# Kernel tuning notes

Hardware: AMD Instinct MI355X
Metric: run time of the kernel (lower is better)

## Reference

```python
import jax, jax.numpy as jnp
import numpy as np

B, C, H, W = 8, 16, 256, 256
HID = 32

def setup_inputs() -> dict:
    key = jax.random.key(0)
    ks = jax.random.split(key, 6)
    swin_logits = jax.random.normal(ks[0], (B, C, H, W), dtype=jnp.float32)
    gru_logits = jax.random.normal(ks[1], (B, C, H, W), dtype=jnp.float32)
    # per-class gate params (stacked across classes); torch Linear default-ish scale
    W1 = jax.random.normal(ks[2], (C, HID, 2), dtype=jnp.float32) * (1.0 / np.sqrt(2.0))
    b1 = jax.random.normal(ks[3], (C, HID), dtype=jnp.float32) * 0.1
    W2 = jax.random.normal(ks[4], (C, 2, HID), dtype=jnp.float32) * (1.0 / np.sqrt(HID))
    b2 = jax.random.normal(ks[5], (C, 2), dtype=jnp.float32) * 0.1
    # expert_preferences initialized exactly as in the torch module
    pref = np.zeros((C, 2), dtype=np.float32)
    for i in range(C):
        w_hls = 0.3 + 0.4 * (i / max(1, C - 1))
        pref[i] = [w_hls, 1.0 - w_hls]
    expert_preferences = jnp.asarray(pref)
    return {"swin_logits": swin_logits, "gru_logits": gru_logits,
            "W1": W1, "b1": b1, "W2": W2, "b2": b2,
            "expert_preferences": expert_preferences}

def reference(swin_logits, gru_logits, W1, b1, W2, b2, expert_preferences):
    b, c, h, w = swin_logits.shape
    # class-dim softmax over logits
    swin_probs = jax.nn.softmax(swin_logits, axis=1)
    gru_probs = jax.nn.softmax(gru_logits, axis=1)
    # (B,C,H,W) -> (N,C), N = B*H*W
    sp = swin_probs.transpose(0, 2, 3, 1).reshape(-1, c)
    gp = gru_probs.transpose(0, 2, 3, 1).reshape(-1, c)
    gate_in = jnp.stack([sp, gp], axis=-1)  # (N, C, 2)
    # batched per-class gate MLP (Dropout is identity in eval mode)
    hid = jax.nn.relu(jnp.einsum('nci,chi->nch', gate_in, W1) + b1)  # (N,C,HID)
    dynamic_weights = jax.nn.softmax(jnp.einsum('nch,coh->nco', hid, W2) + b2, axis=-1)  # (N,C,2)
    # weighted fusion of expert logits
    sl = swin_logits.transpose(0, 2, 3, 1).reshape(-1, c)
    gl = gru_logits.transpose(0, 2, 3, 1).reshape(-1, c)
    expert_logits = jnp.stack([sl, gl], axis=-1)  # (N,C,2)
    fused_flat = jnp.sum(dynamic_weights * expert_logits, axis=-1)  # (N,C)
    fused_logits = fused_flat.reshape(b, h, w, c).transpose(0, 3, 1, 2)
    return fused_logits, expert_preferences, dynamic_weights
```

## Files before the change

kernel.cpp:

```cpp
#include <hip/hip_runtime.h>

typedef float v2f __attribute__((ext_vector_type(2)));

#define Bc   8
#define Cc   16
#define HWc  65536
#define HIDc 32
#define Npix (Bc * HWc)
#define FUSED_ELEMS (Bc * Cc * HWc)
#define PREF_ELEMS  (Cc * 2)
#define TPB  256
#define WSTRIDE 81
#define PACKED_BYTES (Cc * WSTRIDE * 8)

__global__ void gate_prep(const float* __restrict__ W1, const float* __restrict__ b1,
                          const float* __restrict__ W2, const float* __restrict__ b2,
                          v2f* __restrict__ ws)
{
    const int c = blockIdx.x;
    const int j = threadIdx.x;
    v2f* wp = ws + c * WSTRIDE;
    if (j < 16) {
        wp[j]      = (v2f){W1[c*64 + 4*j + 0], W1[c*64 + 4*j + 2]};
        wp[16 + j] = (v2f){W1[c*64 + 4*j + 1], W1[c*64 + 4*j + 3]};
        wp[32 + j] = (v2f){b1[c*32 + 2*j],     b1[c*32 + 2*j + 1]};
        wp[48 + j] = (v2f){W2[c*64 + 2*j],     W2[c*64 + 2*j + 1]};
        wp[64 + j] = (v2f){W2[c*64 + 32 + 2*j],W2[c*64 + 32 + 2*j + 1]};
    } else if (j == 16) {
        wp[80] = (v2f){b2[2*c], b2[2*c + 1]};
    }
}

__global__ __launch_bounds__(TPB)
__attribute__((amdgpu_waves_per_eu(4, 6)))
void gate_main_packed(
    const float* __restrict__ swin, const float* __restrict__ gru,
    const v2f* __restrict__ wsw, const float* __restrict__ pref,
    float* __restrict__ out)
{
    const int tid  = threadIdx.x;
    const int n    = blockIdx.x * TPB + tid;
    const int bidx = n >> 16;
    const int hw   = n & (HWc - 1);

    const float* sptr = swin + (size_t)bidx * (Cc * HWc) + hw;
    const float* gptr = gru  + (size_t)bidx * (Cc * HWc) + hw;

    float sl[Cc], gl[Cc];
#pragma unroll
    for (int c = 0; c < Cc; ++c) {
        sl[c] = sptr[c * HWc];
        gl[c] = gptr[c * HWc];
    }

    float ss0 = 0.f, ss1 = 0.f, sg0 = 0.f, sg1 = 0.f;
#pragma unroll
    for (int c = 0; c < Cc; c += 2) {
        ss0 += __expf(sl[c]);     sg0 += __expf(gl[c]);
        ss1 += __expf(sl[c + 1]); sg1 += __expf(gl[c + 1]);
    }
    const float invs = __builtin_amdgcn_rcpf(ss0 + ss1);
    const float invg = __builtin_amdgcn_rcpf(sg0 + sg1);

    float* fop = out + (size_t)bidx * (Cc * HWc) + hw;

    float dw0[Cc], dw1[Cc];
#pragma unroll
    for (int c = 0; c < Cc; ++c) {
        const float sp = __expf(sl[c]) * invs;
        const float gp = __expf(gl[c]) * invg;
        const v2f spv = {sp, sp};
        const v2f gpv = {gp, gp};

        const v2f* wp = wsw + c * WSTRIDE;

        v2f acc0 = {0.f, 0.f};
        v2f acc1 = {0.f, 0.f};
#pragma unroll
        for (int j = 0; j < HIDc / 2; ++j) {
            v2f h = wp[j] * spv + (wp[16 + j] * gpv + wp[32 + j]);
            h = __builtin_elementwise_max(h, (v2f){0.f, 0.f});
            acc0 = h * wp[48 + j] + acc0;
            acc1 = h * wp[64 + j] + acc1;
        }
        const v2f b2v = wp[80];
        const float a0 = acc0.x + acc0.y + b2v.x;
        const float a1 = acc1.x + acc1.y + b2v.y;

        const float d = a0 - a1;
        const float t = __expf(-fabsf(d));
        const float r = __builtin_amdgcn_rcpf(1.f + t);
        const float w0 = (d >= 0.f) ? r : 1.f - r;
        const float w1 = 1.f - w0;

        fop[c * HWc] = fmaf(w0, sl[c], w1 * gl[c]);
        dw0[c] = w0;
        dw1[c] = w1;
    }

    float4* dwp = reinterpret_cast<float4*>(
        out + (size_t)FUSED_ELEMS + PREF_ELEMS + (size_t)n * (Cc * 2));
#pragma unroll
    for (int k = 0; k < Cc / 2; ++k) {
        dwp[k] = make_float4(dw0[2 * k], dw1[2 * k], dw0[2 * k + 1], dw1[2 * k + 1]);
    }

    if (blockIdx.x == 0 && tid < PREF_ELEMS) {
        out[(size_t)FUSED_ELEMS + tid] = pref[tid];
    }
}

__global__ __launch_bounds__(TPB, 4) void gate_main_scalar(
    const float* __restrict__ swin, const float* __restrict__ gru,
    const float* __restrict__ W1, const float* __restrict__ b1,
    const float* __restrict__ W2, const float* __restrict__ b2,
    const float* __restrict__ pref, float* __restrict__ out)
{
    __shared__ float2 dwbuf2[TPB * Cc];

    const int tid  = threadIdx.x;
    const int n    = blockIdx.x * TPB + tid;
    const int bidx = n >> 16;
    const int hw   = n & (HWc - 1);

    const float* sptr = swin + (size_t)bidx * (Cc * HWc) + hw;
    const float* gptr = gru  + (size_t)bidx * (Cc * HWc) + hw;

    float sl[Cc], gl[Cc];
#pragma unroll
    for (int c = 0; c < Cc; ++c) { sl[c] = sptr[c * HWc]; gl[c] = gptr[c * HWc]; }

    float ms = sl[0], mg = gl[0];
#pragma unroll
    for (int c = 1; c < Cc; ++c) { ms = fmaxf(ms, sl[c]); mg = fmaxf(mg, gl[c]); }
    float es[Cc], eg[Cc];
    float ss = 0.f, sg = 0.f;
#pragma unroll
    for (int c = 0; c < Cc; ++c) {
        es[c] = __expf(sl[c] - ms);  ss += es[c];
        eg[c] = __expf(gl[c] - mg);  sg += eg[c];
    }
    const float invs = __builtin_amdgcn_rcpf(ss);
    const float invg = __builtin_amdgcn_rcpf(sg);

    float* fop = out + (size_t)bidx * (Cc * HWc) + hw;

#pragma unroll
    for (int c = 0; c < Cc; ++c) {
        const float sp = es[c] * invs;
        const float gp = eg[c] * invg;
        const float* w1c = W1 + c * (HIDc * 2);
        const float* b1c = b1 + c * HIDc;
        const float* w2c = W2 + c * (2 * HIDc);

        float a0 = b2[c * 2 + 0];
        float a1 = b2[c * 2 + 1];
#pragma unroll
        for (int k = 0; k < HIDc; ++k) {
            float h = fmaf(w1c[k * 2 + 0], sp, fmaf(w1c[k * 2 + 1], gp, b1c[k]));
            h = fmaxf(h, 0.f);
            a0 = fmaf(w2c[k], h, a0);
            a1 = fmaf(w2c[HIDc + k], h, a1);
        }
        const float d = a0 - a1;
        const float t = __expf(-fabsf(d));
        const float r = __builtin_amdgcn_rcpf(1.f + t);
        const float w0 = (d >= 0.f) ? r : 1.f - r;
        const float w1 = 1.f - w0;

        fop[c * HWc] = fmaf(w0, sl[c], w1 * gl[c]);
        dwbuf2[tid * Cc + ((c + tid) & (Cc - 1))] = make_float2(w0, w1);
    }

    __syncthreads();

    float2* outv2 = reinterpret_cast<float2*>(
        out + (size_t)FUSED_ELEMS + PREF_ELEMS + (size_t)blockIdx.x * (TPB * Cc * 2));
#pragma unroll
    for (int j = 0; j < Cc; ++j) {
        const int pi = j * TPB + tid;
        const int p  = pi >> 4;
        const int pr = pi & (Cc - 1);
        outv2[pi] = dwbuf2[p * Cc + ((pr + p) & (Cc - 1))];
    }

    if (blockIdx.x == 0 && tid < PREF_ELEMS) {
        out[(size_t)FUSED_ELEMS + tid] = pref[tid];
    }
}

extern "C" void kernel_launch(void* const* d_in, const int* in_sizes, int n_in,
                              void* d_out, int out_size, void* d_ws, size_t ws_size,
                              hipStream_t stream) {
    const float* swin = (const float*)d_in[0];
    const float* gru  = (const float*)d_in[1];
    const float* W1   = (const float*)d_in[2];
    const float* b1   = (const float*)d_in[3];
    const float* W2   = (const float*)d_in[4];
    const float* b2   = (const float*)d_in[5];
    const float* pref = (const float*)d_in[6];
    float* out = (float*)d_out;

    dim3 grid(Npix / TPB);
    dim3 block(TPB);

    if (ws_size >= (size_t)PACKED_BYTES) {
        v2f* ws = (v2f*)d_ws;
        hipLaunchKernelGGL(gate_prep, dim3(Cc), dim3(64), 0, stream, W1, b1, W2, b2, ws);
        hipLaunchKernelGGL(gate_main_packed, grid, block, 0, stream,
                           swin, gru, ws, pref, out);
    } else {
        hipLaunchKernelGGL(gate_main_scalar, grid, block, 0, stream,
                           swin, gru, W1, b1, W2, b2, pref, out);
    }
}
```

Measured before the change: 197.3 us.

## Fold 2-way softmax into W2/b2 differences and process two pixels per thread

The gate prep now precomputes the difference of the two output rows of W2 and of b2. The second GEMV then produces the logit difference directly, which halves the second-layer FMAs. The main kernel also handles two adjacent pixels per thread with float2 loads and stores, reusing each weight load across both pixels. The grid is halved and the occupancy hint is pinned to 4 waves/EU, with more register pressure per thread in exchange.

```diff
diff --git a/kernel.cpp b/kernel.cpp
--- a/kernel.cpp
+++ b/kernel.cpp
@@ -10,7 +10,8 @@
 #define FUSED_ELEMS (Bc * Cc * HWc)
 #define PREF_ELEMS  (Cc * 2)
 #define TPB  256
-#define WSTRIDE 81
+#define PIXPT 2
+#define WSTRIDE 65
 #define PACKED_BYTES (Cc * WSTRIDE * 8)
 
 __global__ void gate_prep(const float* __restrict__ W1, const float* __restrict__ b1,
@@ -24,53 +25,59 @@
         wp[j]      = (v2f){W1[c*64 + 4*j + 0], W1[c*64 + 4*j + 2]};
         wp[16 + j] = (v2f){W1[c*64 + 4*j + 1], W1[c*64 + 4*j + 3]};
         wp[32 + j] = (v2f){b1[c*32 + 2*j],     b1[c*32 + 2*j + 1]};
-        wp[48 + j] = (v2f){W2[c*64 + 2*j],     W2[c*64 + 2*j + 1]};
-        wp[64 + j] = (v2f){W2[c*64 + 32 + 2*j],W2[c*64 + 32 + 2*j + 1]};
+        wp[48 + j] = (v2f){W2[c*64 + 2*j]     - W2[c*64 + 32 + 2*j],
+                           W2[c*64 + 2*j + 1] - W2[c*64 + 32 + 2*j + 1]};
     } else if (j == 16) {
-        wp[80] = (v2f){b2[2*c], b2[2*c + 1]};
+        wp[64] = (v2f){b2[2*c] - b2[2*c + 1], 0.f};
     }
 }
 
 __global__ __launch_bounds__(TPB)
-__attribute__((amdgpu_waves_per_eu(4, 6)))
+__attribute__((amdgpu_waves_per_eu(4, 4)))
 void gate_main_packed(
     const float* __restrict__ swin, const float* __restrict__ gru,
     const v2f* __restrict__ wsw, const float* __restrict__ pref,
     float* __restrict__ out)
 {
     const int tid  = threadIdx.x;
-    const int n    = blockIdx.x * TPB + tid;
-    const int bidx = n >> 16;
-    const int hw   = n & (HWc - 1);
+    const int t    = blockIdx.x * TPB + tid;
+    const int p0   = 2 * t;
+    const int bidx = p0 >> 16;
+    const int hw   = p0 & (HWc - 1);
 
     const float* sptr = swin + (size_t)bidx * (Cc * HWc) + hw;
     const float* gptr = gru  + (size_t)bidx * (Cc * HWc) + hw;
 
-    float sl[Cc], gl[Cc];
-#pragma unroll
-    for (int c = 0; c < Cc; ++c) {
-        sl[c] = sptr[c * HWc];
-        gl[c] = gptr[c * HWc];
+    v2f sl[Cc], gl[Cc];
+#pragma unroll
+    for (int c = 0; c < Cc; ++c) {
+        sl[c] = *reinterpret_cast<const v2f*>(sptr + c * HWc);
+        gl[c] = *reinterpret_cast<const v2f*>(gptr + c * HWc);
     }
 
     float ss0 = 0.f, ss1 = 0.f, sg0 = 0.f, sg1 = 0.f;
 #pragma unroll
-    for (int c = 0; c < Cc; c += 2) {
-        ss0 += __expf(sl[c]);     sg0 += __expf(gl[c]);
-        ss1 += __expf(sl[c + 1]); sg1 += __expf(gl[c + 1]);
-    }
-    const float invs = __builtin_amdgcn_rcpf(ss0 + ss1);
-    const float invg = __builtin_amdgcn_rcpf(sg0 + sg1);
+    for (int c = 0; c < Cc; ++c) {
+        ss0 += __expf(sl[c].x);  ss1 += __expf(sl[c].y);
+        sg0 += __expf(gl[c].x);  sg1 += __expf(gl[c].y);
+    }
+    const float invs0 = __builtin_amdgcn_rcpf(ss0);
+    const float invs1 = __builtin_amdgcn_rcpf(ss1);
+    const float invg0 = __builtin_amdgcn_rcpf(sg0);
+    const float invg1 = __builtin_amdgcn_rcpf(sg1);
 
     float* fop = out + (size_t)bidx * (Cc * HWc) + hw;
 
-    float dw0[Cc], dw1[Cc];
-#pragma unroll
-    for (int c = 0; c < Cc; ++c) {
-        const float sp = __expf(sl[c]) * invs;
-        const float gp = __expf(gl[c]) * invg;
-        const v2f spv = {sp, sp};
-        const v2f gpv = {gp, gp};
+    float w0a[Cc], w1a[Cc];
+    float w0b[Cc], w1b[Cc];
+#pragma unroll
+    for (int c = 0; c < Cc; ++c) {
+        const float sp0 = __expf(sl[c].x) * invs0;
+        const float sp1 = __expf(sl[c].y) * invs1;
+        const float gp0 = __expf(gl[c].x) * invg0;
+        const float gp1 = __expf(gl[c].y) * invg1;
+        const v2f sp0v = {sp0, sp0}, sp1v = {sp1, sp1};
+        const v2f gp0v = {gp0, gp0}, gp1v = {gp1, gp1};
 
         const v2f* wp = wsw + c * WSTRIDE;
 
@@ -78,31 +85,48 @@
         v2f acc1 = {0.f, 0.f};
 #pragma unroll
         for (int j = 0; j < HIDc / 2; ++j) {
-            v2f h = wp[j] * spv + (wp[16 + j] * gpv + wp[32 + j]);
-            h = __builtin_elementwise_max(h, (v2f){0.f, 0.f});
-            acc0 = h * wp[48 + j] + acc0;
-            acc1 = h * wp[64 + j] + acc1;
+            const v2f w1s = wp[j];
+            const v2f w1g = wp[16 + j];
+            const v2f b1p = wp[32 + j];
+            const v2f up  = wp[48 + j];
+            v2f h0 = w1s * sp0v + (w1g * gp0v + b1p);
+            v2f h1 = w1s * sp1v + (w1g * gp1v + b1p);
+            h0 = __builtin_elementwise_max(h0, (v2f){0.f, 0.f});
+            h1 = __builtin_elementwise_max(h1, (v2f){0.f, 0.f});
+            acc0 = h0 * up + acc0;
+            acc1 = h1 * up + acc1;
         }
-        const v2f b2v = wp[80];
-        const float a0 = acc0.x + acc0.y + b2v.x;
-        const float a1 = acc1.x + acc1.y + b2v.y;
-
-        const float d = a0 - a1;
-        const float t = __expf(-fabsf(d));
-        const float r = __builtin_amdgcn_rcpf(1.f + t);
-        const float w0 = (d >= 0.f) ? r : 1.f - r;
-        const float w1 = 1.f - w0;
-
-        fop[c * HWc] = fmaf(w0, sl[c], w1 * gl[c]);
-        dw0[c] = w0;
-        dw1[c] = w1;
+        const float e  = wp[64].x;
+        const float d0 = acc0.x + acc0.y + e;
+        const float d1 = acc1.x + acc1.y + e;
+
+        const float t0 = __expf(-fabsf(d0));
+        const float r0 = __builtin_amdgcn_rcpf(1.f + t0);
+        const float w00 = (d0 >= 0.f) ? r0 : 1.f - r0;
+        const float w01 = 1.f - w00;
+        const float t1 = __expf(-fabsf(d1));
+        const float r1 = __builtin_amdgcn_rcpf(1.f + t1);
+        const float w10 = (d1 >= 0.f) ? r1 : 1.f - r1;
+        const float w11 = 1.f - w10;
+
+        v2f fo;
+        fo.x = fmaf(w00, sl[c].x, w01 * gl[c].x);
+        fo.y = fmaf(w10, sl[c].y, w11 * gl[c].y);
+        *reinterpret_cast<v2f*>(fop + c * HWc) = fo;
+
+        w0a[c] = w00; w1a[c] = w01;
+        w0b[c] = w10; w1b[c] = w11;
     }
 
     float4* dwp = reinterpret_cast<float4*>(
-        out + (size_t)FUSED_ELEMS + PREF_ELEMS + (size_t)n * (Cc * 2));
+        out + (size_t)FUSED_ELEMS + PREF_ELEMS + (size_t)p0 * (Cc * 2));
 #pragma unroll
     for (int k = 0; k < Cc / 2; ++k) {
-        dwp[k] = make_float4(dw0[2 * k], dw1[2 * k], dw0[2 * k + 1], dw1[2 * k + 1]);
+        dwp[k] = make_float4(w0a[2*k], w1a[2*k], w0a[2*k + 1], w1a[2*k + 1]);
+    }
+#pragma unroll
+    for (int k = 0; k < Cc / 2; ++k) {
+        dwp[8 + k] = make_float4(w0b[2*k], w1b[2*k], w0b[2*k + 1], w1b[2*k + 1]);
     }
 
     if (blockIdx.x == 0 && tid < PREF_ELEMS) {
@@ -201,16 +225,15 @@
     const float* pref = (const float*)d_in[6];
     float* out = (float*)d_out;
 
-    dim3 grid(Npix / TPB);
     dim3 block(TPB);
 
     if (ws_size >= (size_t)PACKED_BYTES) {
         v2f* ws = (v2f*)d_ws;
         hipLaunchKernelGGL(gate_prep, dim3(Cc), dim3(64), 0, stream, W1, b1, W2, b2, ws);
-        hipLaunchKernelGGL(gate_main_packed, grid, block, 0, stream,
+        hipLaunchKernelGGL(gate_main_packed, dim3(Npix / (TPB * PIXPT)), block, 0, stream,
                            swin, gru, ws, pref, out);
     } else {
-        hipLaunchKernelGGL(gate_main_scalar, grid, block, 0, stream,
+        hipLaunchKernelGGL(gate_main_scalar, dim3(Npix / TPB), block, 0, stream,
                            swin, gru, W1, b1, W2, b2, pref, out);
     }
 }
```

New measurement: 187.9 us. -4.8%, faster.
